# Performance work log

Measured on AMD Instinct MI355X. Metric: run time of the kernel, lower is better.

Reference implementation:

```python
import jax, jax.numpy as jnp
import numpy as np

N = 50000      # nodes
E = 800000     # edges (before self-loops)
IN = 256       # in_channels
OUT = 64       # out_channels per head
H = 4          # heads (layer 0)
LEAKY = 0.2    # PyG GATConv negative_slope default


def setup_inputs() -> dict:
    key = jax.random.key(0)
    ks = jax.random.split(key, 16)
    g = 0.1
    inp = {
        "x": jax.random.normal(ks[0], (N, IN), jnp.float32),
        "edge_index": jax.random.randint(ks[1], (2, E), 0, N, dtype=jnp.int32),
        # layer 0: in -> H*OUT, concat=True
        "W0": jax.random.normal(ks[2], (IN, H * OUT), jnp.float32) * g,
        "a_src0": jax.random.normal(ks[3], (H, OUT), jnp.float32) * g,
        "a_dst0": jax.random.normal(ks[4], (H, OUT), jnp.float32) * g,
        "b0": jnp.zeros((H * OUT,), jnp.float32),
        # layer 1: H*OUT -> OUT, heads=1, concat=False
        "W1": jax.random.normal(ks[5], (H * OUT, OUT), jnp.float32) * g,
        "a_src1": jax.random.normal(ks[6], (1, OUT), jnp.float32) * g,
        "a_dst1": jax.random.normal(ks[7], (1, OUT), jnp.float32) * g,
        "b1": jnp.zeros((OUT,), jnp.float32),
        # layer 2: H*OUT -> OUT (input is OUT from layer 1? no: layer1 outputs OUT)
        "W2": jax.random.normal(ks[8], (OUT, OUT), jnp.float32) * g,
        "a_src2": jax.random.normal(ks[9], (1, OUT), jnp.float32) * g,
        "a_dst2": jax.random.normal(ks[10], (1, OUT), jnp.float32) * g,
        "b2": jnp.zeros((OUT,), jnp.float32),
    }
    return inp


def _gat_layer(x, src, dst, W, a_s, a_d, b, heads, concat):
    """PyG GATConv: per-head linear, edge attention logits, segment softmax
    over incoming edges of each destination node, scatter-sum aggregate."""
    n = x.shape[0]
    h = (x @ W).reshape(n, heads, -1)                      # [N, H, C]
    al_s = (h * a_s).sum(-1)                               # [N, H]
    al_d = (h * a_d).sum(-1)                               # [N, H]
    e = jax.nn.leaky_relu(al_s[src] + al_d[dst], LEAKY)    # [E', H]
    m = jax.ops.segment_max(e, dst, num_segments=n)        # [N, H]
    ex = jnp.exp(e - m[dst])
    den = jax.ops.segment_sum(ex, dst, num_segments=n)     # [N, H]
    alpha = ex / (den[dst] + 1e-16)                        # [E', H]
    out = jax.ops.segment_sum(alpha[:, :, None] * h[src], dst, num_segments=n)  # [N,H,C]
    out = out.reshape(n, -1) if concat else out.mean(axis=1)
    return out + b


def reference(x, edge_index, W0, a_src0, a_dst0, b0, W1, a_src1, a_dst1, b1,
              W2, a_src2, a_dst2, b2):
    n = x.shape[0]
    loop = jnp.arange(n, dtype=edge_index.dtype)
    src = jnp.concatenate([edge_index[0], loop])   # PyG add_self_loops=True
    dst = jnp.concatenate([edge_index[1], loop])
    h = _gat_layer(x, src, dst, W0, a_src0, a_dst0, b0, H, True)
    h = jax.nn.elu(h)
    h = _gat_layer(h, src, dst, W1, a_src1, a_dst1, b1, 1, False)
    h = jax.nn.elu(h)
    h = _gat_layer(h, src, dst, W2, a_src2, a_dst2, b2, 1, False)
    h = jax.nn.elu(h)
    return h
```

## Files before the change

### kernel.cpp

```cpp
#include <hip/hip_runtime.h>
#include <hip/hip_bf16.h>


typedef unsigned short ushort_t;
typedef __attribute__((ext_vector_type(8))) short short8;
typedef __attribute__((ext_vector_type(4))) float f32x4;

__device__ __forceinline__ float elu_f(float x){ return x > 0.f ? x : expm1f(x); }
__device__ __forceinline__ float lrelu_f(float x){ return x > 0.f ? x : 0.2f * x; }
__device__ __forceinline__ ushort_t f2b(float f){
  union { float f; unsigned u; } v; v.f = f;
  unsigned r = v.u + 0x7fff + ((v.u >> 16) & 1);
  return (ushort_t)(r >> 16);
}
__device__ __forceinline__ float b2f_lo(unsigned v){
  union { unsigned u; float f; } c; c.u = v << 16; return c.f;
}
__device__ __forceinline__ float b2f_hi(unsigned v){
  union { unsigned u; float f; } c; c.u = v & 0xffff0000u; return c.f;
}

__global__ __launch_bounds__(256) void prep_kernel(const int* __restrict__ ei,
                                                   int* __restrict__ cnt,
                                                   const float4* __restrict__ x4,
                                                   ushort4* __restrict__ xb4, int n4,
                                                   const float* __restrict__ W0,
                                                   ushort_t* __restrict__ W0p,
                                                   const float* __restrict__ W1,
                                                   ushort_t* __restrict__ W1p,
                                                   const float* __restrict__ W2,
                                                   ushort_t* __restrict__ W2p,
                                                   int E, int Etot, int eb, int fb){
  int bid = blockIdx.x; int t = threadIdx.x;
  if(bid < eb){
    int e = bid * 256 + t;
    if(e < Etot){
      int d = (e < E) ? ei[E + e] : (e - E);
      atomicAdd(&cnt[d], 1);
    }
  } else if(bid < eb + fb){
    int i = (bid - eb) * 256 + t;
    if(i < n4){
      float4 v = x4[i];
      ushort4 o;
      o.x = f2b(v.x); o.y = f2b(v.y); o.z = f2b(v.z); o.w = f2b(v.w);
      xb4[i] = o;
    }
  } else {
    int r = bid - eb - fb;
    if(r < 256){
      int i = r * 256 + t; int k = i >> 8, n = i & 255;
      W0p[(size_t)n * 256 + k] = f2b(W0[i]);
    } else if(r < 320){
      int i = (r - 256) * 256 + t; int k = i >> 6, n = i & 63;
      W1p[(size_t)n * 256 + k] = f2b(W1[i]);
    } else {
      int i = (r - 320) * 256 + t; int k = i >> 6, n = i & 63;
      W2p[(size_t)n * 64 + k] = f2b(W2[i]);
    }
  }
}

__global__ __launch_bounds__(256) void mfma_gemm(const ushort_t* __restrict__ A,
                                                 const ushort_t* __restrict__ Bp,
                                                 ushort_t* __restrict__ Cp,
                                                 const float* __restrict__ asrc,
                                                 const float* __restrict__ adst,
                                                 float* __restrict__ als,
                                                 float* __restrict__ ald,
                                                 int M, int K, int NC){
  int wave = threadIdx.x >> 6;
  int lane = threadIdx.x & 63;
  int tile0 = (blockIdx.x * 4 + wave) * 2;
  if(tile0 * 16 >= M) return;
  bool two = (tile0 + 1) * 16 < M;
  int colb = blockIdx.y;
  int m = lane & 15, q = lane >> 4;
  const ushort_t* Ab = A + (size_t)(tile0 * 16 + m) * K + q * 8;
  const ushort_t* Bq = Bp + (size_t)(colb * 64 + m) * K + q * 8;
  f32x4 acc[2][4] = {};
  for(int k0 = 0; k0 < K; k0 += 32){
    short8 bv[4];
    #pragma unroll
    for(int j = 0; j < 4; j++) bv[j] = *(const short8*)(Bq + (size_t)j * 16 * K + k0);
    short8 a0 = *(const short8*)(Ab + k0);
    #pragma unroll
    for(int j = 0; j < 4; j++)
      acc[0][j] = __builtin_amdgcn_mfma_f32_16x16x32_bf16(a0, bv[j], acc[0][j], 0, 0, 0);
    if(two){
      short8 a1 = *(const short8*)(Ab + (size_t)16 * K + k0);
      #pragma unroll
      for(int j = 0; j < 4; j++)
        acc[1][j] = __builtin_amdgcn_mfma_f32_16x16x32_bf16(a1, bv[j], acc[1][j], 0, 0, 0);
    }
  }
  int hstride = gridDim.y;
  #pragma unroll
  for(int r = 0; r < 2; r++){
    if(r == 1 && !two) break;
    int rowt = tile0 + r;
    #pragma unroll
    for(int j = 0; j < 4; j++){
      int col = colb * 64 + j * 16 + m;
      #pragma unroll
      for(int i = 0; i < 4; i++){
        int rr = rowt * 16 + q * 4 + i;
        Cp[(size_t)rr * NC + col] = f2b(acc[r][j][i]);
      }
    }
    float vs[4] = {0,0,0,0}, vd[4] = {0,0,0,0};
    #pragma unroll
    for(int j = 0; j < 4; j++){
      int col = colb * 64 + j * 16 + m;
      float a_s = asrc[col], a_d = adst[col];
      #pragma unroll
      for(int i = 0; i < 4; i++){
        vs[i] = fmaf(acc[r][j][i], a_s, vs[i]);
        vd[i] = fmaf(acc[r][j][i], a_d, vd[i]);
      }
    }
    #pragma unroll
    for(int off = 8; off > 0; off >>= 1){
      #pragma unroll
      for(int i = 0; i < 4; i++){
        vs[i] += __shfl_down(vs[i], off, 16);
        vd[i] += __shfl_down(vd[i], off, 16);
      }
    }
    if(m == 0){
      #pragma unroll
      for(int i = 0; i < 4; i++){
        int rr = rowt * 16 + q * 4 + i;
        als[(size_t)rr * hstride + colb] = vs[i];
        ald[(size_t)rr * hstride + colb] = vd[i];
      }
    }
  }
}

__global__ __launch_bounds__(256) void blocksum_kernel(const int* __restrict__ cnt,
                                                       int* __restrict__ bsum, int N){
  __shared__ int sm[256];
  int t = threadIdx.x;
  int i = blockIdx.x * 256 + t;
  sm[t] = (i < N) ? cnt[i] : 0;
  __syncthreads();
  for(int off = 128; off > 0; off >>= 1){
    if(t < off) sm[t] += sm[t + off];
    __syncthreads();
  }
  if(t == 0) bsum[blockIdx.x] = sm[0];
}

__global__ __launch_bounds__(256) void scanb_kernel(int* __restrict__ bsum, int nb){
  __shared__ int sm[256];
  int t = threadIdx.x;
  int v = (t < nb) ? bsum[t] : 0;
  sm[t] = v;
  __syncthreads();
  for(int off = 1; off < 256; off <<= 1){
    int x = 0;
    if(t >= off) x = sm[t - off];
    __syncthreads();
    sm[t] += x;
    __syncthreads();
  }
  if(t < nb) bsum[t] = sm[t] - v;
}

__global__ __launch_bounds__(256) void scan2_kernel(const int* __restrict__ cnt,
                                                    const int* __restrict__ bsum,
                                                    int* __restrict__ rowptr,
                                                    int* __restrict__ cursor,
                                                    int N, int Etot){
  __shared__ int sm[256];
  int t = threadIdx.x;
  int i = blockIdx.x * 256 + t;
  int v = (i < N) ? cnt[i] : 0;
  sm[t] = v;
  __syncthreads();
  for(int off = 1; off < 256; off <<= 1){
    int x = 0;
    if(t >= off) x = sm[t - off];
    __syncthreads();
    sm[t] += x;
    __syncthreads();
  }
  if(i < N){
    int ex = sm[t] - v + bsum[blockIdx.x];
    rowptr[i] = ex;
    cursor[i] = ex;
    if(i == N - 1) rowptr[N] = Etot;
  }
}

__global__ __launch_bounds__(256) void scatter_kernel(const int* __restrict__ ei,
                                                      int* __restrict__ cursor,
                                                      int* __restrict__ esrc,
                                                      int E, int Etot){
  int e = blockIdx.x * 256 + threadIdx.x;
  if(e >= Etot) return;
  int s, d;
  if(e < E){ s = ei[e]; d = ei[E + e]; } else { s = e - E; d = s; }
  int pos = atomicAdd(&cursor[d], 1);
  esrc[pos] = s;
}

__global__ __launch_bounds__(256) void agg0_kernel(const int* __restrict__ rowptr,
                                                   const int* __restrict__ esrc,
                                                   const uint2* __restrict__ h0b2,
                                                   const float4* __restrict__ als4,
                                                   const float4* __restrict__ ald4,
                                                   const float4* __restrict__ b4,
                                                   uint2* __restrict__ out2, int N){
  int t = threadIdx.x;
  int lane = t & 63;
  int n = blockIdx.x * 4 + (t >> 6);
  if(n >= N) return;
  int h = lane >> 4;
  int beg = rowptr[n], end = rowptr[n + 1];
  float adh = ((const float*)(ald4 + n))[h];
  float4 acc = make_float4(0.f, 0.f, 0.f, 0.f);
  float den = 0.f;
  for(int c0 = beg; c0 < end; c0 += 16){
    int e = c0 + (lane & 15);
    int s = n; float w = 0.f;
    if(e < end){
      s = esrc[e];
      w = expf(lrelu_f(((const float*)(als4 + s))[h] + adh));
    }
    #pragma unroll
    for(int i = 0; i < 16; i++){
      int idx = (lane & 48) + i;
      int si = __shfl(s, idx, 64);
      float wi = __shfl(w, idx, 64);
      uint2 v = h0b2[((size_t)si << 6) + lane];
      acc.x = fmaf(wi, b2f_lo(v.x), acc.x);
      acc.y = fmaf(wi, b2f_hi(v.x), acc.y);
      acc.z = fmaf(wi, b2f_lo(v.y), acc.z);
      acc.w = fmaf(wi, b2f_hi(v.y), acc.w);
      den += wi;
    }
  }
  float inv = 1.f / (den + 1e-16f);
  float4 bb = b4[lane];
  float v0 = elu_f(acc.x * inv + bb.x);
  float v1 = elu_f(acc.y * inv + bb.y);
  float v2 = elu_f(acc.z * inv + bb.z);
  float v3 = elu_f(acc.w * inv + bb.w);
  uint2 o;
  o.x = (unsigned)f2b(v0) | ((unsigned)f2b(v1) << 16);
  o.y = (unsigned)f2b(v2) | ((unsigned)f2b(v3) << 16);
  out2[((size_t)n << 6) + lane] = o;
}

template<int OMODE>
__global__ __launch_bounds__(256) void agg1_kernel(const int* __restrict__ rowptr,
                                                   const int* __restrict__ esrc,
                                                   const unsigned* __restrict__ gb,
                                                   const float* __restrict__ als,
                                                   const float* __restrict__ ald,
                                                   const float* __restrict__ b,
                                                   void* __restrict__ outp, int N){
  int t = threadIdx.x;
  int lane = t & 63;
  int n = blockIdx.x * 4 + (t >> 6);
  if(n >= N) return;
  int half = lane >> 5;
  int p = lane & 31;
  int beg = rowptr[n], end = rowptr[n + 1];
  float ad = ald[n];
  float a0 = 0.f, a1 = 0.f, den = 0.f;
  for(int c0 = beg; c0 < end; c0 += 32){
    int e = c0 + p;
    int s = n; float w = 0.f;
    if(e < end){
      s = esrc[e];
      w = expf(lrelu_f(als[s] + ad));
    }
    #pragma unroll
    for(int i = 0; i < 16; i++){
      int idx = 2 * i + half;
      int si = __shfl(s, idx, 64);
      float wi = __shfl(w, idx, 64);
      unsigned v = gb[((size_t)si << 5) + p];
      a0 = fmaf(wi, b2f_lo(v), a0);
      a1 = fmaf(wi, b2f_hi(v), a1);
      den += wi;
    }
  }
  a0 += __shfl_xor(a0, 32, 64);
  a1 += __shfl_xor(a1, 32, 64);
  den += __shfl_xor(den, 32, 64);
  float inv = 1.f / (den + 1e-16f);
  float2 bb = ((const float2*)b)[p];
  float v0 = elu_f(a0 * inv + bb.x);
  float v1 = elu_f(a1 * inv + bb.y);
  if(half == 0){
    if(OMODE == 0){
      ((unsigned*)outp)[((size_t)n << 5) + p] =
          (unsigned)f2b(v0) | ((unsigned)f2b(v1) << 16);
    } else {
      float2 o; o.x = v0; o.y = v1;
      ((float2*)outp)[((size_t)n << 5) + p] = o;
    }
  }
}

extern "C" void kernel_launch(void* const* d_in, const int* in_sizes, int n_in,
                              void* d_out, int out_size, void* d_ws, size_t ws_size,
                              hipStream_t stream){
  const float* x   = (const float*)d_in[0];
  const int*   ei  = (const int*)d_in[1];
  const float* W0  = (const float*)d_in[2];
  const float* as0 = (const float*)d_in[3];
  const float* ad0 = (const float*)d_in[4];
  const float* b0  = (const float*)d_in[5];
  const float* W1  = (const float*)d_in[6];
  const float* as1 = (const float*)d_in[7];
  const float* ad1 = (const float*)d_in[8];
  const float* b1  = (const float*)d_in[9];
  const float* W2  = (const float*)d_in[10];
  const float* as2 = (const float*)d_in[11];
  const float* ad2 = (const float*)d_in[12];
  const float* b2  = (const float*)d_in[13];
  int N = in_sizes[0] / 256;
  int E = in_sizes[1] / 2;
  int Etot = E + N;

  size_t off = 0;
  auto alc = [&](size_t bytes) -> char* {
    char* p = (char*)d_ws + off;
    off += (bytes + 255) & ~(size_t)255;
    return p;
  };
  ushort_t* xb    = (ushort_t*)alc((size_t)N * 256 * 2);
  ushort_t* h0b   = (ushort_t*)alc((size_t)N * 256 * 2);
  float*    als   = (float*)alc((size_t)N * 4 * 4);
  float*    ald   = (float*)alc((size_t)N * 4 * 4);
  int*      esrc  = (int*)alc((size_t)Etot * 4);
  int*      rowptr= (int*)alc((size_t)(N + 1) * 4);
  int*      cnt   = (int*)alc((size_t)N * 4);
  int*      cursor= (int*)alc((size_t)N * 4);
  int*      bsum  = (int*)alc(256 * 4);
  ushort_t* W0p   = (ushort_t*)alc(256 * 256 * 2);
  ushort_t* W1p   = (ushort_t*)alc(256 * 64 * 2);
  ushort_t* W2p   = (ushort_t*)alc(64 * 64 * 2);

  ushort_t* h1b = xb;
  ushort_t* h2b = xb;
  ushort_t* g1b = h0b;
  ushort_t* g2b = h0b;

  int nb = (N + 255) / 256;
  int eb = (Etot + 255) / 256;
  int fb = (N * 64 + 255) / 256;
  int rb = ((N / 16) + 7) / 8;
  int ab = (N + 3) / 4;

  hipMemsetAsync(cnt, 0, (size_t)N * 4, stream);
  prep_kernel<<<eb + fb + 336, 256, 0, stream>>>(ei, cnt, (const float4*)x,
                                                 (ushort4*)xb, N * 64,
                                                 W0, W0p, W1, W1p, W2, W2p,
                                                 E, Etot, eb, fb);
  blocksum_kernel<<<nb, 256, 0, stream>>>(cnt, bsum, N);
  scanb_kernel<<<1, 256, 0, stream>>>(bsum, nb);
  scan2_kernel<<<nb, 256, 0, stream>>>(cnt, bsum, rowptr, cursor, N, Etot);
  scatter_kernel<<<eb, 256, 0, stream>>>(ei, cursor, esrc, E, Etot);

  mfma_gemm<<<dim3(rb, 4), 256, 0, stream>>>(xb, W0p, h0b, as0, ad0,
                                             als, ald, N, 256, 256);
  agg0_kernel<<<ab, 256, 0, stream>>>(rowptr, esrc, (const uint2*)h0b,
                                      (const float4*)als, (const float4*)ald,
                                      (const float4*)b0, (uint2*)h1b, N);

  mfma_gemm<<<dim3(rb, 1), 256, 0, stream>>>(h1b, W1p, g1b, as1, ad1,
                                             als, ald, N, 256, 64);
  agg1_kernel<0><<<ab, 256, 0, stream>>>(rowptr, esrc, (const unsigned*)g1b,
                                         als, ald, b1, h2b, N);

  mfma_gemm<<<dim3(rb, 1), 256, 0, stream>>>(h2b, W2p, g2b, as2, ad2,
                                             als, ald, N, 64, 64);
  agg1_kernel<1><<<ab, 256, 0, stream>>>(rowptr, esrc, (const unsigned*)g2b,
                                         als, ald, b2, d_out, N);
}
```

Baseline: 391.5 us.

## Fuse aggregation with next layer GEMM and stage A tiles in LDS

```diff
diff --git a/kernel.cpp b/kernel.cpp
--- a/kernel.cpp
+++ b/kernel.cpp
@@ -61,51 +61,58 @@
   }
 }
 
-__global__ __launch_bounds__(256) void mfma_gemm(const ushort_t* __restrict__ A,
-                                                 const ushort_t* __restrict__ Bp,
-                                                 ushort_t* __restrict__ Cp,
-                                                 const float* __restrict__ asrc,
-                                                 const float* __restrict__ adst,
-                                                 float* __restrict__ als,
-                                                 float* __restrict__ ald,
-                                                 int M, int K, int NC){
-  int wave = threadIdx.x >> 6;
-  int lane = threadIdx.x & 63;
-  int tile0 = (blockIdx.x * 4 + wave) * 2;
-  if(tile0 * 16 >= M) return;
-  bool two = (tile0 + 1) * 16 < M;
-  int colb = blockIdx.y;
+#define SKP 264
+__global__ __launch_bounds__(256) void gemm0_kernel(const ushort_t* __restrict__ A,
+                                                    const ushort_t* __restrict__ Bp,
+                                                    ushort_t* __restrict__ h0b,
+                                                    const float* __restrict__ asrc,
+                                                    const float* __restrict__ adst,
+                                                    float* __restrict__ als,
+                                                    float* __restrict__ ald, int M){
+  __shared__ ushort_t As[32 * SKP];
+  int t = threadIdx.x;
+  int row0 = blockIdx.x * 32;
+  {
+    int c = t;
+    #pragma unroll
+    for(int it = 0; it < 4; it++, c += 256){
+      int r = c >> 5;
+      int kc = (c & 31) << 3;
+      int gr = row0 + r;
+      short8 v = {};
+      if(gr < M) v = *(const short8*)(A + (size_t)gr * 256 + kc);
+      *(short8*)(As + r * SKP + kc) = v;
+    }
+  }
+  __syncthreads();
+  int wave = t >> 6, lane = t & 63;
   int m = lane & 15, q = lane >> 4;
-  const ushort_t* Ab = A + (size_t)(tile0 * 16 + m) * K + q * 8;
-  const ushort_t* Bq = Bp + (size_t)(colb * 64 + m) * K + q * 8;
+  int colb = wave;
+  const ushort_t* Bq = Bp + (size_t)(colb * 64 + m) * 256 + q * 8;
+  const ushort_t* A0 = As + m * SKP + q * 8;
+  const ushort_t* A1 = As + (16 + m) * SKP + q * 8;
   f32x4 acc[2][4] = {};
-  for(int k0 = 0; k0 < K; k0 += 32){
+  for(int k0 = 0; k0 < 256; k0 += 32){
     short8 bv[4];
     #pragma unroll
-    for(int j = 0; j < 4; j++) bv[j] = *(const short8*)(Bq + (size_t)j * 16 * K + k0);
-    short8 a0 = *(const short8*)(Ab + k0);
-    #pragma unroll
-    for(int j = 0; j < 4; j++)
+    for(int j = 0; j < 4; j++) bv[j] = *(const short8*)(Bq + (size_t)j * 16 * 256 + k0);
+    short8 a0 = *(const short8*)(A0 + k0);
+    short8 a1 = *(const short8*)(A1 + k0);
+    #pragma unroll
+    for(int j = 0; j < 4; j++){
       acc[0][j] = __builtin_amdgcn_mfma_f32_16x16x32_bf16(a0, bv[j], acc[0][j], 0, 0, 0);
-    if(two){
-      short8 a1 = *(const short8*)(Ab + (size_t)16 * K + k0);
-      #pragma unroll
-      for(int j = 0; j < 4; j++)
-        acc[1][j] = __builtin_amdgcn_mfma_f32_16x16x32_bf16(a1, bv[j], acc[1][j], 0, 0, 0);
-    }
-  }
-  int hstride = gridDim.y;
-  #pragma unroll
-  for(int r = 0; r < 2; r++){
-    if(r == 1 && !two) break;
-    int rowt = tile0 + r;
+      acc[1][j] = __builtin_amdgcn_mfma_f32_16x16x32_bf16(a1, bv[j], acc[1][j], 0, 0, 0);
+    }
+  }
+  #pragma unroll
+  for(int rt = 0; rt < 2; rt++){
     #pragma unroll
     for(int j = 0; j < 4; j++){
       int col = colb * 64 + j * 16 + m;
       #pragma unroll
       for(int i = 0; i < 4; i++){
-        int rr = rowt * 16 + q * 4 + i;
-        Cp[(size_t)rr * NC + col] = f2b(acc[r][j][i]);
+        int gr = row0 + rt * 16 + q * 4 + i;
+        if(gr < M) h0b[(size_t)gr * 256 + col] = f2b(acc[rt][j][i]);
       }
     }
     float vs[4] = {0,0,0,0}, vd[4] = {0,0,0,0};
@@ -115,8 +122,8 @@
       float a_s = asrc[col], a_d = adst[col];
       #pragma unroll
       for(int i = 0; i < 4; i++){
-        vs[i] = fmaf(acc[r][j][i], a_s, vs[i]);
-        vd[i] = fmaf(acc[r][j][i], a_d, vd[i]);
+        vs[i] = fmaf(acc[rt][j][i], a_s, vs[i]);
+        vd[i] = fmaf(acc[rt][j][i], a_d, vd[i]);
       }
     }
     #pragma unroll
@@ -130,9 +137,11 @@
     if(m == 0){
       #pragma unroll
       for(int i = 0; i < 4; i++){
-        int rr = rowt * 16 + q * 4 + i;
-        als[(size_t)rr * hstride + colb] = vs[i];
-        ald[(size_t)rr * hstride + colb] = vd[i];
+        int gr = row0 + rt * 16 + q * 4 + i;
+        if(gr < M){
+          als[(size_t)gr * 4 + colb] = vs[i];
+          ald[(size_t)gr * 4 + colb] = vd[i];
+        }
       }
     }
   }
@@ -206,62 +215,218 @@
   esrc[pos] = s;
 }
 
-__global__ __launch_bounds__(256) void agg0_kernel(const int* __restrict__ rowptr,
-                                                   const int* __restrict__ esrc,
-                                                   const uint2* __restrict__ h0b2,
-                                                   const float4* __restrict__ als4,
-                                                   const float4* __restrict__ ald4,
-                                                   const float4* __restrict__ b4,
-                                                   uint2* __restrict__ out2, int N){
-  int t = threadIdx.x;
-  int lane = t & 63;
-  int n = blockIdx.x * 4 + (t >> 6);
-  if(n >= N) return;
+#define H1S 264
+__global__ __launch_bounds__(256) void agg0g1_kernel(const int* __restrict__ rowptr,
+                                                     const int* __restrict__ esrc,
+                                                     const uint2* __restrict__ h0b2,
+                                                     const float* __restrict__ als,
+                                                     const float* __restrict__ ald,
+                                                     const float* __restrict__ b0,
+                                                     const ushort_t* __restrict__ W1p,
+                                                     const float* __restrict__ as1,
+                                                     const float* __restrict__ ad1,
+                                                     ushort_t* __restrict__ g1b,
+                                                     float* __restrict__ als1,
+                                                     float* __restrict__ ald1, int N){
+  __shared__ ushort_t Hs[16 * H1S];
+  __shared__ float aps[4][16], apd[4][16];
+  int t = threadIdx.x;
+  int wave = t >> 6, lane = t & 63;
+  int nbase = blockIdx.x * 16;
   int h = lane >> 4;
-  int beg = rowptr[n], end = rowptr[n + 1];
-  float adh = ((const float*)(ald4 + n))[h];
-  float4 acc = make_float4(0.f, 0.f, 0.f, 0.f);
-  float den = 0.f;
-  for(int c0 = beg; c0 < end; c0 += 16){
-    int e = c0 + (lane & 15);
-    int s = n; float w = 0.f;
-    if(e < end){
-      s = esrc[e];
-      w = expf(lrelu_f(((const float*)(als4 + s))[h] + adh));
-    }
-    #pragma unroll
-    for(int i = 0; i < 16; i++){
-      int idx = (lane & 48) + i;
-      int si = __shfl(s, idx, 64);
-      float wi = __shfl(w, idx, 64);
-      uint2 v = h0b2[((size_t)si << 6) + lane];
-      acc.x = fmaf(wi, b2f_lo(v.x), acc.x);
-      acc.y = fmaf(wi, b2f_hi(v.x), acc.y);
-      acc.z = fmaf(wi, b2f_lo(v.y), acc.z);
-      acc.w = fmaf(wi, b2f_hi(v.y), acc.w);
-      den += wi;
-    }
-  }
-  float inv = 1.f / (den + 1e-16f);
-  float4 bb = b4[lane];
-  float v0 = elu_f(acc.x * inv + bb.x);
-  float v1 = elu_f(acc.y * inv + bb.y);
-  float v2 = elu_f(acc.z * inv + bb.z);
-  float v3 = elu_f(acc.w * inv + bb.w);
-  uint2 o;
-  o.x = (unsigned)f2b(v0) | ((unsigned)f2b(v1) << 16);
-  o.y = (unsigned)f2b(v2) | ((unsigned)f2b(v3) << 16);
-  out2[((size_t)n << 6) + lane] = o;
-}
-
-template<int OMODE>
-__global__ __launch_bounds__(256) void agg1_kernel(const int* __restrict__ rowptr,
+  int mm16 = lane & 15;
+  for(int j = 0; j < 4; j++){
+    int n = nbase + wave * 4 + j;
+    int nl = wave * 4 + j;
+    if(n < N){
+      int beg = rowptr[n], end = rowptr[n + 1];
+      float adh = ald[(size_t)n * 4 + h];
+      float4 acc = make_float4(0.f, 0.f, 0.f, 0.f);
+      float den = 0.f;
+      for(int c0 = beg; c0 < end; c0 += 16){
+        int e = c0 + mm16;
+        int s = n; float w = 0.f;
+        if(e < end){
+          s = esrc[e];
+          w = expf(lrelu_f(als[(size_t)s * 4 + h] + adh));
+        }
+        #pragma unroll
+        for(int i = 0; i < 16; i++){
+          int idx = (lane & 48) + i;
+          int si = __shfl(s, idx, 64);
+          float wi = __shfl(w, idx, 64);
+          uint2 v = h0b2[((size_t)si << 6) + lane];
+          acc.x = fmaf(wi, b2f_lo(v.x), acc.x);
+          acc.y = fmaf(wi, b2f_hi(v.x), acc.y);
+          acc.z = fmaf(wi, b2f_lo(v.y), acc.z);
+          acc.w = fmaf(wi, b2f_hi(v.y), acc.w);
+          den += wi;
+        }
+      }
+      float inv = 1.f / (den + 1e-16f);
+      float4 bb = ((const float4*)b0)[lane];
+      uint2 o;
+      o.x = (unsigned)f2b(elu_f(acc.x * inv + bb.x)) |
+            ((unsigned)f2b(elu_f(acc.y * inv + bb.y)) << 16);
+      o.y = (unsigned)f2b(elu_f(acc.z * inv + bb.z)) |
+            ((unsigned)f2b(elu_f(acc.w * inv + bb.w)) << 16);
+      *(uint2*)(Hs + nl * H1S + lane * 4) = o;
+    }
+  }
+  __syncthreads();
+  int m = lane & 15, q = lane >> 4;
+  const ushort_t* Bw = W1p + (size_t)(wave * 16 + m) * 256 + q * 8;
+  const ushort_t* Aw = Hs + m * H1S + q * 8;
+  f32x4 acc = {};
+  #pragma unroll
+  for(int k0 = 0; k0 < 256; k0 += 32){
+    short8 av = *(const short8*)(Aw + k0);
+    short8 bv = *(const short8*)(Bw + k0);
+    acc = __builtin_amdgcn_mfma_f32_16x16x32_bf16(av, bv, acc, 0, 0, 0);
+  }
+  float a_s = as1[wave * 16 + m], a_d = ad1[wave * 16 + m];
+  float vs[4], vd[4];
+  #pragma unroll
+  for(int i = 0; i < 4; i++){
+    int gn = nbase + q * 4 + i;
+    if(gn < N) g1b[(size_t)gn * 64 + wave * 16 + m] = f2b(acc[i]);
+    vs[i] = acc[i] * a_s;
+    vd[i] = acc[i] * a_d;
+  }
+  #pragma unroll
+  for(int off = 8; off > 0; off >>= 1){
+    #pragma unroll
+    for(int i = 0; i < 4; i++){
+      vs[i] += __shfl_down(vs[i], off, 16);
+      vd[i] += __shfl_down(vd[i], off, 16);
+    }
+  }
+  if(m == 0){
+    #pragma unroll
+    for(int i = 0; i < 4; i++){
+      aps[wave][q * 4 + i] = vs[i];
+      apd[wave][q * 4 + i] = vd[i];
+    }
+  }
+  __syncthreads();
+  if(t < 16){
+    int gn = nbase + t;
+    if(gn < N){
+      als1[gn] = aps[0][t] + aps[1][t] + aps[2][t] + aps[3][t];
+      ald1[gn] = apd[0][t] + apd[1][t] + apd[2][t] + apd[3][t];
+    }
+  }
+}
+
+#define H2S 72
+__global__ __launch_bounds__(256) void agg1g2_kernel(const int* __restrict__ rowptr,
+                                                     const int* __restrict__ esrc,
+                                                     const unsigned* __restrict__ g1b,
+                                                     const float* __restrict__ als1,
+                                                     const float* __restrict__ ald1,
+                                                     const float* __restrict__ b1,
+                                                     const ushort_t* __restrict__ W2p,
+                                                     const float* __restrict__ as2,
+                                                     const float* __restrict__ ad2,
+                                                     ushort_t* __restrict__ g2b,
+                                                     float* __restrict__ als2,
+                                                     float* __restrict__ ald2, int N){
+  __shared__ ushort_t Hs[16 * H2S];
+  __shared__ float aps[4][16], apd[4][16];
+  int t = threadIdx.x;
+  int wave = t >> 6, lane = t & 63;
+  int nbase = blockIdx.x * 16;
+  int half = lane >> 5;
+  int p = lane & 31;
+  for(int j = 0; j < 4; j++){
+    int n = nbase + wave * 4 + j;
+    int nl = wave * 4 + j;
+    if(n < N){
+      int beg = rowptr[n], end = rowptr[n + 1];
+      float ad = ald1[n];
+      float a0 = 0.f, a1 = 0.f, den = 0.f;
+      for(int c0 = beg; c0 < end; c0 += 32){
+        int e = c0 + p;
+        int s = n; float w = 0.f;
+        if(e < end){
+          s = esrc[e];
+          w = expf(lrelu_f(als1[s] + ad));
+        }
+        #pragma unroll
+        for(int i = 0; i < 16; i++){
+          int idx = 2 * i + half;
+          int si = __shfl(s, idx, 64);
+          float wi = __shfl(w, idx, 64);
+          unsigned v = g1b[((size_t)si << 5) + p];
+          a0 = fmaf(wi, b2f_lo(v), a0);
+          a1 = fmaf(wi, b2f_hi(v), a1);
+          den += wi;
+        }
+      }
+      a0 += __shfl_xor(a0, 32, 64);
+      a1 += __shfl_xor(a1, 32, 64);
+      den += __shfl_xor(den, 32, 64);
+      float inv = 1.f / (den + 1e-16f);
+      float2 bb = ((const float2*)b1)[p];
+      if(half == 0){
+        unsigned o = (unsigned)f2b(elu_f(a0 * inv + bb.x)) |
+                     ((unsigned)f2b(elu_f(a1 * inv + bb.y)) << 16);
+        *(unsigned*)(Hs + nl * H2S + p * 2) = o;
+      }
+    }
+  }
+  __syncthreads();
+  int m = lane & 15, q = lane >> 4;
+  const ushort_t* Bw = W2p + (size_t)(wave * 16 + m) * 64 + q * 8;
+  const ushort_t* Aw = Hs + m * H2S + q * 8;
+  f32x4 acc = {};
+  #pragma unroll
+  for(int k0 = 0; k0 < 64; k0 += 32){
+    short8 av = *(const short8*)(Aw + k0);
+    short8 bv = *(const short8*)(Bw + k0);
+    acc = __builtin_amdgcn_mfma_f32_16x16x32_bf16(av, bv, acc, 0, 0, 0);
+  }
+  float a_s = as2[wave * 16 + m], a_d = ad2[wave * 16 + m];
+  float vs[4], vd[4];
+  #pragma unroll
+  for(int i = 0; i < 4; i++){
+    int gn = nbase + q * 4 + i;
+    if(gn < N) g2b[(size_t)gn * 64 + wave * 16 + m] = f2b(acc[i]);
+    vs[i] = acc[i] * a_s;
+    vd[i] = acc[i] * a_d;
+  }
+  #pragma unroll
+  for(int off = 8; off > 0; off >>= 1){
+    #pragma unroll
+    for(int i = 0; i < 4; i++){
+      vs[i] += __shfl_down(vs[i], off, 16);
+      vd[i] += __shfl_down(vd[i], off, 16);
+    }
+  }
+  if(m == 0){
+    #pragma unroll
+    for(int i = 0; i < 4; i++){
+      aps[wave][q * 4 + i] = vs[i];
+      apd[wave][q * 4 + i] = vd[i];
+    }
+  }
+  __syncthreads();
+  if(t < 16){
+    int gn = nbase + t;
+    if(gn < N){
+      als2[gn] = aps[0][t] + aps[1][t] + aps[2][t] + aps[3][t];
+      ald2[gn] = apd[0][t] + apd[1][t] + apd[2][t] + apd[3][t];
+    }
+  }
+}
+
+__global__ __launch_bounds__(256) void aggF_kernel(const int* __restrict__ rowptr,
                                                    const int* __restrict__ esrc,
                                                    const unsigned* __restrict__ gb,
                                                    const float* __restrict__ als,
                                                    const float* __restrict__ ald,
                                                    const float* __restrict__ b,
-                                                   void* __restrict__ outp, int N){
+                                                   float2* __restrict__ outp, int N){
   int t = threadIdx.x;
   int lane = t & 63;
   int n = blockIdx.x * 4 + (t >> 6);
@@ -294,16 +459,11 @@
   den += __shfl_xor(den, 32, 64);
   float inv = 1.f / (den + 1e-16f);
   float2 bb = ((const float2*)b)[p];
-  float v0 = elu_f(a0 * inv + bb.x);
-  float v1 = elu_f(a1 * inv + bb.y);
   if(half == 0){
-    if(OMODE == 0){
-      ((unsigned*)outp)[((size_t)n << 5) + p] =
-          (unsigned)f2b(v0) | ((unsigned)f2b(v1) << 16);
-    } else {
-      float2 o; o.x = v0; o.y = v1;
-      ((float2*)outp)[((size_t)n << 5) + p] = o;
-    }
+    float2 o;
+    o.x = elu_f(a0 * inv + bb.x);
+    o.y = elu_f(a1 * inv + bb.y);
+    outp[((size_t)n << 5) + p] = o;
   }
 }
 
@@ -338,6 +498,10 @@
   ushort_t* h0b   = (ushort_t*)alc((size_t)N * 256 * 2);
   float*    als   = (float*)alc((size_t)N * 4 * 4);
   float*    ald   = (float*)alc((size_t)N * 4 * 4);
+  float*    als1  = (float*)alc((size_t)N * 4);
+  float*    ald1  = (float*)alc((size_t)N * 4);
+  float*    als2  = (float*)alc((size_t)N * 4);
+  float*    ald2  = (float*)alc((size_t)N * 4);
   int*      esrc  = (int*)alc((size_t)Etot * 4);
   int*      rowptr= (int*)alc((size_t)(N + 1) * 4);
   int*      cnt   = (int*)alc((size_t)N * 4);
@@ -347,15 +511,14 @@
   ushort_t* W1p   = (ushort_t*)alc(256 * 64 * 2);
   ushort_t* W2p   = (ushort_t*)alc(64 * 64 * 2);
 
-  ushort_t* h1b = xb;
-  ushort_t* h2b = xb;
-  ushort_t* g1b = h0b;
+  ushort_t* g1b = xb;
   ushort_t* g2b = h0b;
 
   int nb = (N + 255) / 256;
   int eb = (Etot + 255) / 256;
   int fb = (N * 64 + 255) / 256;
-  int rb = ((N / 16) + 7) / 8;
+  int g0b = (N + 31) / 32;
+  int tb = (N + 15) / 16;
   int ab = (N + 3) / 4;
 
   hipMemsetAsync(cnt, 0, (size_t)N * 4, stream);
@@ -368,19 +531,16 @@
   scan2_kernel<<<nb, 256, 0, stream>>>(cnt, bsum, rowptr, cursor, N, Etot);
   scatter_kernel<<<eb, 256, 0, stream>>>(ei, cursor, esrc, E, Etot);
 
-  mfma_gemm<<<dim3(rb, 4), 256, 0, stream>>>(xb, W0p, h0b, as0, ad0,
-                                             als, ald, N, 256, 256);
-  agg0_kernel<<<ab, 256, 0, stream>>>(rowptr, esrc, (const uint2*)h0b,
-                                      (const float4*)als, (const float4*)ald,
-                                      (const float4*)b0, (uint2*)h1b, N);
-
-  mfma_gemm<<<dim3(rb, 1), 256, 0, stream>>>(h1b, W1p, g1b, as1, ad1,
-                                             als, ald, N, 256, 64);
-  agg1_kernel<0><<<ab, 256, 0, stream>>>(rowptr, esrc, (const unsigned*)g1b,
-                                         als, ald, b1, h2b, N);
-
-  mfma_gemm<<<dim3(rb, 1), 256, 0, stream>>>(h2b, W2p, g2b, as2, ad2,
-                                             als, ald, N, 64, 64);
-  agg1_kernel<1><<<ab, 256, 0, stream>>>(rowptr, esrc, (const unsigned*)g2b,
-                                         als, ald, b2, d_out, N);
-}
+  gemm0_kernel<<<g0b, 256, 0, stream>>>(xb, W0p, h0b, as0, ad0, als, ald, N);
+
+  agg0g1_kernel<<<tb, 256, 0, stream>>>(rowptr, esrc, (const uint2*)h0b,
+                                        als, ald, b0, W1p, as1, ad1,
+                                        g1b, als1, ald1, N);
+
+  agg1g2_kernel<<<tb, 256, 0, stream>>>(rowptr, esrc, (const unsigned*)g1b,
+                                        als1, ald1, b1, W2p, as2, ad2,
+                                        g2b, als2, ald2, N);
+
+  aggF_kernel<<<ab, 256, 0, stream>>>(rowptr, esrc, (const unsigned*)g2b,
+                                      als2, ald2, b2, (float2*)d_out, N);
+}
```

Result: faster. 379.2 us (-3.2%).
